# Kernel tuning notes

Measured on AMD Instinct MI355X. Metric: run time of the kernel, lower is better.

Reference implementation:

```python
import jax, jax.numpy as jnp
import numpy as np

B, T, D_IN, H, V = 512, 128, 128, 256, 50257


def _lstm_layer(x, Wih, Whh, bih, bhh):
    """Single LSTM layer, PyTorch gate order (i, f, g, o). x: [B, T, D]."""
    bsz = x.shape[0]
    hid = Whh.shape[1]
    b = bih + bhh  # fuse the two bias adds once

    def step(carry, xt):
        h, c = carry
        gates = xt @ Wih.T + h @ Whh.T + b  # [B, 4H]
        i, f, g, o = jnp.split(gates, 4, axis=-1)
        i = jax.nn.sigmoid(i)
        f = jax.nn.sigmoid(f)
        g = jnp.tanh(g)
        o = jax.nn.sigmoid(o)
        c = f * c + i * g
        h = o * jnp.tanh(c)
        return (h, c), h

    h0 = jnp.zeros((bsz, hid), x.dtype)
    (_, _), hs = jax.lax.scan(step, (h0, h0), jnp.swapaxes(x, 0, 1))  # hs: [T, B, H]
    return jnp.swapaxes(hs, 0, 1)  # [B, T, H]


def setup_inputs() -> dict:
    key = jax.random.key(0)
    ks = jax.random.split(key, 12)
    s = 1.0 / np.sqrt(H)  # torch LSTM/Linear default init scale
    inp = {
        "x": jax.random.normal(ks[0], (B, T, D_IN), dtype=jnp.float32),
        "Wih0": jax.random.uniform(ks[1], (4 * H, D_IN), jnp.float32, -s, s),
        "Whh0": jax.random.uniform(ks[2], (4 * H, H), jnp.float32, -s, s),
        "bih0": jax.random.uniform(ks[3], (4 * H,), jnp.float32, -s, s),
        "bhh0": jax.random.uniform(ks[4], (4 * H,), jnp.float32, -s, s),
        "Wih1": jax.random.uniform(ks[5], (4 * H, H), jnp.float32, -s, s),
        "Whh1": jax.random.uniform(ks[6], (4 * H, H), jnp.float32, -s, s),
        "bih1": jax.random.uniform(ks[7], (4 * H,), jnp.float32, -s, s),
        "bhh1": jax.random.uniform(ks[8], (4 * H,), jnp.float32, -s, s),
        "fcW": jax.random.uniform(ks[9], (V, H), jnp.float32, -s, s),
        "fcb": jax.random.uniform(ks[10], (V,), jnp.float32, -s, s),
    }
    return inp


def reference(x, Wih0, Whh0, bih0, bhh0, Wih1, Whh1, bih1, bhh1, fcW, fcb):
    h = _lstm_layer(x, Wih0, Whh0, bih0, bhh0)   # [B, T, H]
    h = _lstm_layer(h, Wih1, Whh1, bih1, bhh1)   # [B, T, H]
    # dropout(p=0.2) in eval mode == identity (deterministic reference)
    last = h[:, -1, :]                            # [B, H]
    logits = last @ fcW.T + fcb                   # [B, V]
    return jax.nn.softmax(logits, axis=-1)
```

## Files before the change

kernel.cpp:

```cpp
#include <hip/hip_runtime.h>
#include <hip/hip_bf16.h>

__device__ __forceinline__ float bf2f(unsigned short u) {
    union { unsigned int i; float f; } x; x.i = ((unsigned int)u) << 16; return x.f;
}
__device__ __forceinline__ unsigned short f2bf(float f) {
    union { float f; unsigned int i; } x; x.f = f;
    unsigned int r = x.i + 0x7fffu + ((x.i >> 16) & 1u);
    return (unsigned short)(r >> 16);
}
__device__ __forceinline__ float sigm(float x) { return 1.0f / (1.0f + __expf(-x)); }
__device__ __forceinline__ float ftanh(float x) {
    x = fminf(15.f, fmaxf(-15.f, x));
    float t = __expf(2.0f * x);
    return (t - 1.0f) / (t + 1.0f);
}

typedef __attribute__((ext_vector_type(8))) short bf16x8;
typedef __attribute__((ext_vector_type(4))) float f32x4;

__device__ __forceinline__ bf16x8 pack8(float4 a, float4 b) {
    bf16x8 v;
    v[0] = (short)f2bf(a.x); v[1] = (short)f2bf(a.y);
    v[2] = (short)f2bf(a.z); v[3] = (short)f2bf(a.w);
    v[4] = (short)f2bf(b.x); v[5] = (short)f2bf(b.y);
    v[6] = (short)f2bf(b.z); v[7] = (short)f2bf(b.w);
    return v;
}

__global__ __launch_bounds__(256) void cvt_f32_bf16(
    const float* __restrict__ in, unsigned short* __restrict__ out, int n8)
{
    int i = blockIdx.x * 256 + threadIdx.x;
    if (i >= n8) return;
    float4 a = *(const float4*)(in + (size_t)i * 8);
    float4 b = *(const float4*)(in + (size_t)i * 8 + 4);
    *(bf16x8*)(out + (size_t)i * 8) = pack8(a, b);
}

__global__ __launch_bounds__(256) void cvt_x_transpose(
    const float* __restrict__ in, unsigned short* __restrict__ out)
{
    int c = blockIdx.x * 256 + threadIdx.x;
    int b = c >> 11, t = (c >> 4) & 127, kc = c & 15;
    const float* src = in + (((size_t)b * 128 + t) * 16 + kc) * 8;
    float4 a = *(const float4*)src;
    float4 bb = *(const float4*)(src + 4);
    *(bf16x8*)(out + (((size_t)t * 512 + b) * 16 + kc) * 8) = pack8(a, bb);
}

template<int K, bool OUT_BF16, bool GUARD_N>
__global__ __launch_bounds__(256) void gemm_mfma(
    const unsigned short* __restrict__ A,
    const unsigned short* __restrict__ Bm,
    const float* __restrict__ bias0,
    const float* __restrict__ bias1,
    void* __restrict__ Cptr, long ldC, int N)
{
    constexpr int LDA = 72;
    __shared__ unsigned short As[128 * LDA];
    __shared__ unsigned short Bs[128 * LDA];
    const int tid = threadIdx.x;
    const int lane = tid & 63;
    const int l15 = lane & 15, lg = lane >> 4;
    const int wid = tid >> 6;
    const int wr = wid >> 1, wc = wid & 1;
    const int m0 = blockIdx.y * 128, n0 = blockIdx.x * 128;
    const int srow = tid >> 3;
    const int scol = (tid & 7) * 8;

    f32x4 acc[4][4];
    #pragma unroll
    for (int mi = 0; mi < 4; ++mi)
        #pragma unroll
        for (int ni = 0; ni < 4; ++ni)
            acc[mi][ni] = (f32x4){0.f, 0.f, 0.f, 0.f};

    for (int kt = 0; kt < K / 64; ++kt) {
        bf16x8 avals[4], bvals[4];
        #pragma unroll
        for (int i = 0; i < 4; ++i) {
            avals[i] = *(const bf16x8*)(A + (size_t)(m0 + i * 32 + srow) * K + kt * 64 + scol);
            int brow = n0 + i * 32 + srow;
            if (GUARD_N) brow = (brow < N) ? brow : (N - 1);
            bvals[i] = *(const bf16x8*)(Bm + (size_t)brow * K + kt * 64 + scol);
        }
        __syncthreads();
        #pragma unroll
        for (int i = 0; i < 4; ++i) {
            *(bf16x8*)&As[(i * 32 + srow) * LDA + scol] = avals[i];
            *(bf16x8*)&Bs[(i * 32 + srow) * LDA + scol] = bvals[i];
        }
        __syncthreads();
        #pragma unroll
        for (int ks = 0; ks < 2; ++ks) {
            bf16x8 af[4], bf[4];
            #pragma unroll
            for (int mi = 0; mi < 4; ++mi)
                af[mi] = *(const bf16x8*)&As[(wr * 64 + mi * 16 + l15) * LDA + ks * 32 + lg * 8];
            #pragma unroll
            for (int ni = 0; ni < 4; ++ni)
                bf[ni] = *(const bf16x8*)&Bs[(wc * 64 + ni * 16 + l15) * LDA + ks * 32 + lg * 8];
            #pragma unroll
            for (int mi = 0; mi < 4; ++mi)
                #pragma unroll
                for (int ni = 0; ni < 4; ++ni)
                    acc[mi][ni] = __builtin_amdgcn_mfma_f32_16x16x32_bf16(
                        af[mi], bf[ni], acc[mi][ni], 0, 0, 0);
        }
    }

    #pragma unroll
    for (int ni = 0; ni < 4; ++ni) {
        int n = n0 + wc * 64 + ni * 16 + l15;
        bool nok = (!GUARD_N) || (n < N);
        float bsum = 0.f;
        if (nok) { bsum = bias0[n]; if (bias1) bsum += bias1[n]; }
        #pragma unroll
        for (int mi = 0; mi < 4; ++mi) {
            int m = m0 + wr * 64 + mi * 16 + lg * 4;
            #pragma unroll
            for (int r = 0; r < 4; ++r) {
                float v = acc[mi][ni][r] + bsum;
                if (nok) {
                    if (OUT_BF16)
                        ((unsigned short*)Cptr)[(size_t)(m + r) * ldC + n] = f2bf(v);
                    else
                        ((float*)Cptr)[(size_t)(m + r) * ldC + n] = v;
                }
            }
        }
    }
}

#define RFRAGS 46
#define LFRAGS 18
#define LDS_HBYTES 8448
#define LDS_TOTAL (LDS_HBYTES + LFRAGS * 8 * 1024)

__global__ __launch_bounds__(512, 2) void lstm_persist(
    const unsigned short* __restrict__ G,
    const float* __restrict__ Whh,
    unsigned short* __restrict__ h0out,
    unsigned short* __restrict__ hlast)
{
    extern __shared__ char smem[];
    char* ldsW = smem + LDS_HBYTES;

    const int lid = threadIdx.x;
    const int w = lid >> 6;
    const int l = lid & 63;
    const int l15 = l & 15, lg = l >> 4;
    const int bc = blockIdx.x;

    bf16x8 wreg[RFRAGS];
    #pragma unroll
    for (int f = 0; f < RFRAGS; ++f) {
        const int cg = f >> 5, type = (f >> 3) & 3, ks = f & 7;
        const int grow = type * 256 + w * 32 + cg * 16 + l15;
        const int k0 = ks * 32 + lg * 8;
        const float* src = Whh + (size_t)grow * 256 + k0;
        wreg[f] = pack8(*(const float4*)src, *(const float4*)(src + 4));
    }
    for (int f = RFRAGS; f < 64; ++f) {
        const int cg = f >> 5, type = (f >> 3) & 3, ks = f & 7;
        const int grow = type * 256 + w * 32 + cg * 16 + l15;
        const int k0 = ks * 32 + lg * 8;
        const float* src = Whh + (size_t)grow * 256 + k0;
        *(bf16x8*)(ldsW + (size_t)(w * LFRAGS + (f - RFRAGS)) * 1024 + l * 16) =
            pack8(*(const float4*)src, *(const float4*)(src + 4));
    }

    for (int i = lid; i < 16 * 264; i += 512) ((unsigned short*)smem)[i] = 0;
    __syncthreads();

    float cst[2][4] = {};
    unsigned short hb16[2][4];

    for (int t = 0; t < 128; ++t) {
        const unsigned short* Gt = G + ((size_t)t * 512 + bc * 16) * 1024;

        #pragma unroll
        for (int cg = 0; cg < 2; ++cg) {
            unsigned short gv[4][4];
            #pragma unroll
            for (int type = 0; type < 4; ++type)
                #pragma unroll
                for (int r = 0; r < 4; ++r)
                    gv[type][r] = Gt[(size_t)(lg * 4 + r) * 1024
                                     + type * 256 + w * 32 + cg * 16 + l15];

            f32x4 acc[4];
            #pragma unroll
            for (int type = 0; type < 4; ++type) acc[type] = (f32x4){0.f, 0.f, 0.f, 0.f};

            #pragma unroll
            for (int ks = 0; ks < 8; ++ks) {
                bf16x8 a = *(const bf16x8*)(smem + l15 * 528 + ks * 64 + lg * 16);
                #pragma unroll
                for (int type = 0; type < 4; ++type) {
                    const int f = cg * 32 + type * 8 + ks;
                    bf16x8 b;
                    if (f < RFRAGS) b = wreg[f];
                    else b = *(const bf16x8*)(ldsW + (w * LFRAGS + (f - RFRAGS)) * 1024 + l * 16);
                    acc[type] = __builtin_amdgcn_mfma_f32_16x16x32_bf16(a, b, acc[type], 0, 0, 0);
                }
            }

            #pragma unroll
            for (int r = 0; r < 4; ++r) {
                float p0 = acc[0][r] + bf2f(gv[0][r]);
                float p1 = acc[1][r] + bf2f(gv[1][r]);
                float p2 = acc[2][r] + bf2f(gv[2][r]);
                float p3 = acc[3][r] + bf2f(gv[3][r]);
                float ii = sigm(p0), ff = sigm(p1), gg = ftanh(p2), oo = sigm(p3);
                float cn = ff * cst[cg][r] + ii * gg;
                cst[cg][r] = cn;
                float hn = oo * ftanh(cn);
                hb16[cg][r] = f2bf(hn);
                if (h0out)
                    h0out[((size_t)t * 512 + bc * 16 + lg * 4 + r) * 256
                          + w * 32 + cg * 16 + l15] = hb16[cg][r];
                if (hlast && t == 127)
                    hlast[(size_t)(bc * 16 + lg * 4 + r) * 256
                          + w * 32 + cg * 16 + l15] = hb16[cg][r];
            }
        }

        __syncthreads();
        #pragma unroll
        for (int cg = 0; cg < 2; ++cg)
            #pragma unroll
            for (int r = 0; r < 4; ++r)
                *(unsigned short*)(smem + (lg * 4 + r) * 528
                                   + (w * 32 + cg * 16 + l15) * 2) = hb16[cg][r];
        __syncthreads();
    }
}

__global__ __launch_bounds__(256) void softmax_rows(
    const float* __restrict__ logits, float* __restrict__ out)
{
    const int b = blockIdx.x;
    const int lid = threadIdx.x;
    const float* row = logits + (size_t)b * 50257;
    __shared__ float red[256];

    float m = -3.4e38f;
    for (int v = lid; v < 50257; v += 256) m = fmaxf(m, row[v]);
    red[lid] = m; __syncthreads();
    for (int s = 128; s > 0; s >>= 1) {
        if (lid < s) red[lid] = fmaxf(red[lid], red[lid + s]);
        __syncthreads();
    }
    m = red[0]; __syncthreads();

    float sum = 0.f;
    for (int v = lid; v < 50257; v += 256) sum += __expf(row[v] - m);
    red[lid] = sum; __syncthreads();
    for (int s = 128; s > 0; s >>= 1) {
        if (lid < s) red[lid] += red[lid + s];
        __syncthreads();
    }
    float inv = 1.0f / red[0];

    float* orow = out + (size_t)b * 50257;
    for (int v = lid; v < 50257; v += 256) orow[v] = __expf(row[v] - m) * inv;
}

extern "C" void kernel_launch(void* const* d_in, const int* in_sizes, int n_in,
                              void* d_out, int out_size, void* d_ws, size_t ws_size,
                              hipStream_t stream) {
    (void)in_sizes; (void)n_in; (void)out_size; (void)ws_size;
    const float* x    = (const float*)d_in[0];
    const float* Wih0 = (const float*)d_in[1];
    const float* Whh0 = (const float*)d_in[2];
    const float* bih0 = (const float*)d_in[3];
    const float* bhh0 = (const float*)d_in[4];
    const float* Wih1 = (const float*)d_in[5];
    const float* Whh1 = (const float*)d_in[6];
    const float* bih1 = (const float*)d_in[7];
    const float* bhh1 = (const float*)d_in[8];
    const float* fcW  = (const float*)d_in[9];
    const float* fcb  = (const float*)d_in[10];
    float* out = (float*)d_out;

    char* ws = (char*)d_ws;
    unsigned short* G      = (unsigned short*)ws;
    unsigned short* h0all  = (unsigned short*)(ws + 134217728);
    unsigned short* xb     = h0all;
    char* misc             = ws + 167772160;
    unsigned short* W0b    = (unsigned short*)(misc);
    unsigned short* W1b    = (unsigned short*)(misc + 262144);
    unsigned short* hlastb = (unsigned short*)(misc + 786432);
    float* logits          = (float*)ws;
    unsigned short* fcWb   = (unsigned short*)(ws + 103809024);

    static bool attr_set = false;
    if (!attr_set) {
        hipFuncSetAttribute((const void*)lstm_persist,
                            hipFuncAttributeMaxDynamicSharedMemorySize, LDS_TOTAL);
        attr_set = true;
    }

    cvt_x_transpose<<<4096, 256, 0, stream>>>(x, xb);
    cvt_f32_bf16<<<64, 256, 0, stream>>>(Wih0, W0b, 16384);
    gemm_mfma<128, true, false><<<dim3(8, 512), 256, 0, stream>>>(
        xb, W0b, bih0, bhh0, G, 1024, 1024);
    lstm_persist<<<32, 512, LDS_TOTAL, stream>>>(G, Whh0, h0all, nullptr);
    cvt_f32_bf16<<<128, 256, 0, stream>>>(Wih1, W1b, 32768);
    gemm_mfma<256, true, false><<<dim3(8, 512), 256, 0, stream>>>(
        h0all, W1b, bih1, bhh1, G, 1024, 1024);
    lstm_persist<<<32, 512, LDS_TOTAL, stream>>>(G, Whh1, nullptr, hlastb);
    cvt_f32_bf16<<<6283, 256, 0, stream>>>(fcW, fcWb, 1608224);
    gemm_mfma<256, false, true><<<dim3(393, 4), 256, 0, stream>>>(
        hlastb, fcWb, fcb, nullptr, logits, 50257, 50257);
    softmax_rows<<<512, 256, 0, stream>>>(logits, out);
}
```

Measured before the change: 1.999 ms.

## Prefetch next-step LSTM gate inputs with permuted packed layout and lighter barriers

The input-projection GEMM now writes its output with a column permutation, so each lane can fetch the gate values for both of its column groups in a single 32-bit load. The persistent LSTM kernel double-buffers these gate values in registers and issues the next timestep's global loads before the current step's MFMAs, taking global memory latency off the serial recurrence. The two __syncthreads per step become an explicit lgkmcnt wait plus s_barrier. It costs more registers, and on the final step it reads one timestep past the end of the gate buffer.

```diff
diff --git a/kernel.cpp b/kernel.cpp
--- a/kernel.cpp
+++ b/kernel.cpp
@@ -49,7 +49,7 @@
     *(bf16x8*)(out + (((size_t)t * 512 + b) * 16 + kc) * 8) = pack8(a, bb);
 }
 
-template<int K, bool OUT_BF16, bool GUARD_N>
+template<int K, bool OUT_BF16, bool GUARD_N, bool PERM>
 __global__ __launch_bounds__(256) void gemm_mfma(
     const unsigned short* __restrict__ A,
     const unsigned short* __restrict__ Bm,
@@ -116,6 +116,7 @@
         bool nok = (!GUARD_N) || (n < N);
         float bsum = 0.f;
         if (nok) { bsum = bias0[n]; if (bias1) bsum += bias1[n]; }
+        int ns = PERM ? ((n & ~31) | ((n & 15) << 1) | ((n >> 4) & 1)) : n;
         #pragma unroll
         for (int mi = 0; mi < 4; ++mi) {
             int m = m0 + wr * 64 + mi * 16 + lg * 4;
@@ -124,9 +125,9 @@
                 float v = acc[mi][ni][r] + bsum;
                 if (nok) {
                     if (OUT_BF16)
-                        ((unsigned short*)Cptr)[(size_t)(m + r) * ldC + n] = f2bf(v);
+                        ((unsigned short*)Cptr)[(size_t)(m + r) * ldC + ns] = f2bf(v);
                     else
-                        ((float*)Cptr)[(size_t)(m + r) * ldC + n] = v;
+                        ((float*)Cptr)[(size_t)(m + r) * ldC + ns] = v;
                 }
             }
         }
@@ -137,6 +138,80 @@
 #define LFRAGS 18
 #define LDS_HBYTES 8448
 #define LDS_TOTAL (LDS_HBYTES + LFRAGS * 8 * 1024)
+
+__device__ __forceinline__ void lstm_step_body(
+    int t, const unsigned short* __restrict__ G, size_t gbase,
+    unsigned int* __restrict__ cur, unsigned int* __restrict__ nxt,
+    char* __restrict__ smem, char* __restrict__ ldsW,
+    const bf16x8* __restrict__ wreg, float (*__restrict__ cst)[4],
+    int w, int l, int l15, int lg, int bc,
+    unsigned short* __restrict__ h0out, unsigned short* __restrict__ hlast)
+{
+    const unsigned short* Gn = G + ((size_t)(t + 1) * 512 * 1024) + gbase;
+    #pragma unroll
+    for (int ty = 0; ty < 4; ++ty)
+        #pragma unroll
+        for (int r = 0; r < 4; ++r)
+            nxt[ty * 4 + r] = *(const unsigned int*)(Gn + ty * 256 + (size_t)r * 1024);
+
+    unsigned short hb16[2][4];
+    #pragma unroll
+    for (int cg = 0; cg < 2; ++cg) {
+        f32x4 acc[4];
+        #pragma unroll
+        for (int ty = 0; ty < 4; ++ty) acc[ty] = (f32x4){0.f, 0.f, 0.f, 0.f};
+
+        #pragma unroll
+        for (int ks = 0; ks < 8; ++ks) {
+            bf16x8 a = *(const bf16x8*)(smem + l15 * 528 + ks * 64 + lg * 16);
+            #pragma unroll
+            for (int ty = 0; ty < 4; ++ty) {
+                const int f = cg * 32 + ty * 8 + ks;
+                bf16x8 b;
+                if (f < RFRAGS) b = wreg[f];
+                else b = *(const bf16x8*)(ldsW + (w * LFRAGS + (f - RFRAGS)) * 1024 + l * 16);
+                acc[ty] = __builtin_amdgcn_mfma_f32_16x16x32_bf16(a, b, acc[ty], 0, 0, 0);
+            }
+        }
+
+        #pragma unroll
+        for (int r = 0; r < 4; ++r) {
+            float pre[4];
+            #pragma unroll
+            for (int ty = 0; ty < 4; ++ty) {
+                unsigned int p = cur[ty * 4 + r];
+                unsigned short g16 = (cg == 0) ? (unsigned short)(p & 0xffffu)
+                                               : (unsigned short)(p >> 16);
+                pre[ty] = acc[ty][r] + bf2f(g16);
+            }
+            float ii = sigm(pre[0]), ff = sigm(pre[1]);
+            float gg = ftanh(pre[2]), oo = sigm(pre[3]);
+            float cn = ff * cst[cg][r] + ii * gg;
+            cst[cg][r] = cn;
+            float hn = oo * ftanh(cn);
+            hb16[cg][r] = f2bf(hn);
+            if (h0out)
+                h0out[((size_t)t * 512 + bc * 16 + lg * 4 + r) * 256
+                      + w * 32 + cg * 16 + l15] = hb16[cg][r];
+            if (hlast && t == 127)
+                hlast[(size_t)(bc * 16 + lg * 4 + r) * 256
+                      + w * 32 + cg * 16 + l15] = hb16[cg][r];
+        }
+    }
+
+    asm volatile("s_waitcnt lgkmcnt(0)" ::: "memory");
+    __builtin_amdgcn_s_barrier();
+
+    #pragma unroll
+    for (int cg = 0; cg < 2; ++cg)
+        #pragma unroll
+        for (int r = 0; r < 4; ++r)
+            *(unsigned short*)(smem + (lg * 4 + r) * 528
+                               + (w * 32 + cg * 16 + l15) * 2) = hb16[cg][r];
+
+    asm volatile("s_waitcnt lgkmcnt(0)" ::: "memory");
+    __builtin_amdgcn_s_barrier();
+}
 
 __global__ __launch_bounds__(512, 2) void lstm_persist(
     const unsigned short* __restrict__ G,
@@ -175,66 +250,25 @@
     __syncthreads();
 
     float cst[2][4] = {};
-    unsigned short hb16[2][4];
-
-    for (int t = 0; t < 128; ++t) {
-        const unsigned short* Gt = G + ((size_t)t * 512 + bc * 16) * 1024;
-
-        #pragma unroll
-        for (int cg = 0; cg < 2; ++cg) {
-            unsigned short gv[4][4];
-            #pragma unroll
-            for (int type = 0; type < 4; ++type)
-                #pragma unroll
-                for (int r = 0; r < 4; ++r)
-                    gv[type][r] = Gt[(size_t)(lg * 4 + r) * 1024
-                                     + type * 256 + w * 32 + cg * 16 + l15];
-
-            f32x4 acc[4];
-            #pragma unroll
-            for (int type = 0; type < 4; ++type) acc[type] = (f32x4){0.f, 0.f, 0.f, 0.f};
-
-            #pragma unroll
-            for (int ks = 0; ks < 8; ++ks) {
-                bf16x8 a = *(const bf16x8*)(smem + l15 * 528 + ks * 64 + lg * 16);
-                #pragma unroll
-                for (int type = 0; type < 4; ++type) {
-                    const int f = cg * 32 + type * 8 + ks;
-                    bf16x8 b;
-                    if (f < RFRAGS) b = wreg[f];
-                    else b = *(const bf16x8*)(ldsW + (w * LFRAGS + (f - RFRAGS)) * 1024 + l * 16);
-                    acc[type] = __builtin_amdgcn_mfma_f32_16x16x32_bf16(a, b, acc[type], 0, 0, 0);
-                }
-            }
-
-            #pragma unroll
-            for (int r = 0; r < 4; ++r) {
-                float p0 = acc[0][r] + bf2f(gv[0][r]);
-                float p1 = acc[1][r] + bf2f(gv[1][r]);
-                float p2 = acc[2][r] + bf2f(gv[2][r]);
-                float p3 = acc[3][r] + bf2f(gv[3][r]);
-                float ii = sigm(p0), ff = sigm(p1), gg = ftanh(p2), oo = sigm(p3);
-                float cn = ff * cst[cg][r] + ii * gg;
-                cst[cg][r] = cn;
-                float hn = oo * ftanh(cn);
-                hb16[cg][r] = f2bf(hn);
-                if (h0out)
-                    h0out[((size_t)t * 512 + bc * 16 + lg * 4 + r) * 256
-                          + w * 32 + cg * 16 + l15] = hb16[cg][r];
-                if (hlast && t == 127)
-                    hlast[(size_t)(bc * 16 + lg * 4 + r) * 256
-                          + w * 32 + cg * 16 + l15] = hb16[cg][r];
-            }
-        }
-
-        __syncthreads();
-        #pragma unroll
-        for (int cg = 0; cg < 2; ++cg)
+    unsigned int gvA[16], gvB[16];
+
+    const size_t gbase = (size_t)bc * 16 * 1024 + (size_t)lg * 4 * 1024
+                       + w * 32 + l15 * 2;
+
+    {
+        const unsigned short* G0 = G + gbase;
+        #pragma unroll
+        for (int ty = 0; ty < 4; ++ty)
             #pragma unroll
             for (int r = 0; r < 4; ++r)
-                *(unsigned short*)(smem + (lg * 4 + r) * 528
-                                   + (w * 32 + cg * 16 + l15) * 2) = hb16[cg][r];
-        __syncthreads();
+                gvA[ty * 4 + r] = *(const unsigned int*)(G0 + ty * 256 + (size_t)r * 1024);
+    }
+
+    for (int t = 0; t < 128; t += 2) {
+        lstm_step_body(t,     G, gbase, gvA, gvB, smem, ldsW, wreg, cst,
+                       w, l, l15, lg, bc, h0out, hlast);
+        lstm_step_body(t + 1, G, gbase, gvB, gvA, smem, ldsW, wreg, cst,
+                       w, l, l15, lg, bc, h0out, hlast);
     }
 }
 
@@ -305,15 +339,15 @@
 
     cvt_x_transpose<<<4096, 256, 0, stream>>>(x, xb);
     cvt_f32_bf16<<<64, 256, 0, stream>>>(Wih0, W0b, 16384);
-    gemm_mfma<128, true, false><<<dim3(8, 512), 256, 0, stream>>>(
+    gemm_mfma<128, true, false, true><<<dim3(8, 512), 256, 0, stream>>>(
         xb, W0b, bih0, bhh0, G, 1024, 1024);
     lstm_persist<<<32, 512, LDS_TOTAL, stream>>>(G, Whh0, h0all, nullptr);
     cvt_f32_bf16<<<128, 256, 0, stream>>>(Wih1, W1b, 32768);
-    gemm_mfma<256, true, false><<<dim3(8, 512), 256, 0, stream>>>(
+    gemm_mfma<256, true, false, true><<<dim3(8, 512), 256, 0, stream>>>(
         h0all, W1b, bih1, bhh1, G, 1024, 1024);
     lstm_persist<<<32, 512, LDS_TOTAL, stream>>>(G, Whh1, nullptr, hlastb);
     cvt_f32_bf16<<<6283, 256, 0, stream>>>(fcW, fcWb, 1608224);
-    gemm_mfma<256, false, true><<<dim3(393, 4), 256, 0, stream>>>(
+    gemm_mfma<256, false, true, false><<<dim3(393, 4), 256, 0, stream>>>(
         hlastb, fcWb, fcb, nullptr, logits, 50257, 50257);
     softmax_rows<<<512, 256, 0, stream>>>(logits, out);
 }
```

New measurement: 2.337 ms. 16.9% more time.
